# Kernel tuning notes

Hardware: AMD Instinct MI355X
Metric: run time of the kernel (lower is better)

Reference implementation:

```python
import jax, jax.numpy as jnp
import numpy as np

# Dimensions
B, C, H, W = 4, 256, 64, 64
O = 256                      # out_channels
K = 3                        # kernel size
K2 = K * K
STRIDE = (1, 1)
PAD = 1
Ho = (H + 2 * PAD - K) // STRIDE[0] + 1   # 64
Wo = (W + 2 * PAD - K) // STRIDE[1] + 1   # 64


def setup_inputs() -> dict:
    key = jax.random.key(0)
    ks = jax.random.split(key, 5)
    x = jax.random.normal(ks[0], (B, C, H, W), jnp.float32)
    # NOTE: the torch module zero-inits offset/modulator convs; we use small
    # random weights so the deformable sampling path is actually exercised.
    offset_w = 0.02 * jax.random.normal(ks[1], (2 * K2, C, K, K), jnp.float32)
    offset_b = jnp.zeros((2 * K2,), jnp.float32)
    mod_w = 0.02 * jax.random.normal(ks[2], (K2, C, K, K), jnp.float32)
    mod_b = jnp.zeros((K2,), jnp.float32)
    weight = jax.random.normal(ks[3], (O, C, K, K), jnp.float32) / np.sqrt(C * K2)
    return {"x": x, "offset_w": offset_w, "offset_b": offset_b,
            "mod_w": mod_w, "mod_b": mod_b, "weight": weight}


def _conv(x, w, b):
    y = jax.lax.conv_general_dilated(
        x, w, window_strides=STRIDE, padding=[(PAD, PAD), (PAD, PAD)],
        dimension_numbers=("NCHW", "OIHW", "NCHW"))
    return y + b[None, :, None, None]


def _deform_conv2d(x, offset, mask, weight):
    """Modulated deformable conv v2 (torchvision semantics, zero padding)."""
    Bq, Cq, Hq, Wq = x.shape
    # offset channels are (dy, dx) pairs per kernel tap, row-major over kernel
    off = offset.reshape(Bq, K2, 2, Ho, Wo)
    ky, kx = jnp.meshgrid(jnp.arange(K), jnp.arange(K), indexing="ij")
    ky = ky.reshape(K2).astype(x.dtype)
    kx = kx.reshape(K2).astype(x.dtype)
    hy = (jnp.arange(Ho) * STRIDE[0] - PAD).astype(x.dtype)
    wx = (jnp.arange(Wo) * STRIDE[1] - PAD).astype(x.dtype)
    # sampling positions [B, K2, Ho, Wo]
    py = off[:, :, 0] + ky[None, :, None, None] + hy[None, None, :, None]
    px = off[:, :, 1] + kx[None, :, None, None] + wx[None, None, None, :]

    P = K2 * Ho * Wo
    xf = x.reshape(Bq, Cq, Hq * Wq)
    y0 = jnp.floor(py)
    x0 = jnp.floor(px)
    val = jnp.zeros((Bq, Cq, P), x.dtype)
    for dy in (0.0, 1.0):
        for dx in (0.0, 1.0):
            yc = y0 + dy
            xc = x0 + dx
            wgt = (1.0 - jnp.abs(py - yc)) * (1.0 - jnp.abs(px - xc))
            valid = (yc >= 0) & (yc < Hq) & (xc >= 0) & (xc < Wq)
            idx = (jnp.clip(yc, 0, Hq - 1) * Wq
                   + jnp.clip(xc, 0, Wq - 1)).astype(jnp.int32).reshape(Bq, P)
            g = jnp.take_along_axis(xf, idx[:, None, :], axis=2)  # [B,C,P]
            val = val + (wgt * valid.astype(x.dtype)).reshape(Bq, 1, P) * g
    # modulation mask is per kernel tap, shared across channels
    cols = (val * mask.reshape(Bq, 1, P)).reshape(Bq, Cq, K2, Ho * Wo)
    out = jnp.einsum("bckp,ock->bop", cols, weight.reshape(weight.shape[0], Cq, K2))
    return out.reshape(Bq, weight.shape[0], Ho, Wo)


def reference(x, offset_w, offset_b, mod_w, mod_b, weight):
    offset = _conv(x, offset_w, offset_b)
    mask = 2.0 * jax.nn.sigmoid(_conv(x, mod_w, mod_b))
    return _deform_conv2d(x, offset, mask, weight)
```

## Files before the change

kernel.cpp:

```cpp
#include <hip/hip_runtime.h>
#include <math.h>


constexpr int Bn = 4;
constexpr int Cn = 256;
constexpr int Hn = 64;
constexpr int Wn = 64;
constexpr int On = 256;
constexpr int PB = Hn * Wn;
constexpr int NCH = 27;

typedef __attribute__((ext_vector_type(8))) _Float16 f16x8;
typedef __attribute__((ext_vector_type(2))) _Float16 f16x2;
typedef __attribute__((ext_vector_type(4))) float f32x4;

union FragU { uint4 u; f16x8 h; };

__device__ inline ushort f2h(float f) {
    _Float16 h = (_Float16)f;
    return __builtin_bit_cast(ushort, h);
}
__device__ inline uint pkh(float a, float b) {
    return __builtin_bit_cast(uint, __builtin_amdgcn_cvt_pkrtz(a, b));
}
__device__ inline f16x2 u2h(uint u) { return __builtin_bit_cast(f16x2, u); }
__device__ inline uint h2u(f16x2 h) { return __builtin_bit_cast(uint, h); }

__global__ __launch_bounds__(256)
void nhwcpack_kernel(const float* __restrict__ x,
                     const float* __restrict__ w,
                     const float* __restrict__ offw,
                     const float* __restrict__ modw,
                     ushort* __restrict__ xhf,
                     ushort* __restrict__ wTb,
                     ushort* __restrict__ owf)
{
    const int bid = blockIdx.x;
    const int b = bid >> 7, seg = bid & 127;
    const int t = threadIdx.x;
    __shared__ float tile[32][257];

    const float* src = x + (size_t)b * Cn * PB + seg * 32;
    #pragma unroll 4
    for (int i = 0; i < 32; ++i) {
        const int idx = i * 256 + t;
        const int c = idx >> 5, p = idx & 31;
        tile[p][c] = src[(size_t)c * PB + p];
    }
    __syncthreads();

    const int pr = t & 127;
    const int r0 = (t >> 7) * 16;
    uint* dH = reinterpret_cast<uint*>(xhf + ((size_t)b * PB + seg * 32) * 256);
    #pragma unroll 4
    for (int i = 0; i < 16; ++i) {
        const int row = r0 + i;
        const float v0 = tile[row][2 * pr];
        const float v1 = tile[row][2 * pr + 1];
        dH[(size_t)row * 128 + pr] = pkh(v0, v1);
    }

    #pragma unroll 1
    for (int u = 0; u < 5; ++u) {
        int unit = (u < 4) ? bid * 4 + u : (bid < 256 ? 2048 + bid : -1);
        if (unit < 0) break;
        const int tap = unit >> 8, c = unit & 255;
        const int o = t;
        wTb[((size_t)(unit >> 3) * 256 + o) * 8 + (c & 7)] =
            f2h(w[((size_t)o * Cn + c) * 9 + tap]);
        if (o < 32) {
            float v = 0.f;
            if (o < 18)      v = offw[((size_t)o * Cn + c) * 9 + tap];
            else if (o < 27) v = modw[((size_t)(o - 18) * Cn + c) * 9 + tap];
            owf[((size_t)(unit >> 3) * 32 + o) * 8 + (c & 7)] = f2h(v);
        }
    }
}

__global__ __launch_bounds__(512, 1)
void offmask_tile_kernel(const ushort* __restrict__ xhf,
                         const float* __restrict__ offb,
                         const float* __restrict__ modb,
                         const ushort* __restrict__ owf,
                         float* __restrict__ offm)
{
    const int hw = blockIdx.x;
    const int blk = (hw & 7) * 32 + (hw >> 3);
    const int b = blk >> 6, row = blk & 63;
    const int t = threadIdx.x;
    const int lane = t & 63;
    const int wv  = t >> 6;
    const int l15 = lane & 15;
    const int g   = lane >> 4;
    const int mt  = wv >> 2;
    const int nt  = wv & 3;

    __shared__ ushort xt[3 * 66 * 256];
    uint4* lds4 = reinterpret_cast<uint4*>(xt);

    {
        const int c  = t >> 3;
        const int og = (t & 7) * 4;
        #pragma unroll 1
        for (int r = 0; r < 3; ++r) {
            const int ysrc = row - 1 + r;
            const int ci = c + 1;
            const int base = (r * 66 + ci) * 32;
            if (ysrc >= 0 && ysrc < Hn) {
                const uint4* src = reinterpret_cast<const uint4*>(
                    xhf + ((size_t)(b * PB + ysrc * 64 + c)) * 256);
                #pragma unroll
                for (int j = 0; j < 4; ++j) {
                    const int o = og + j;
                    lds4[base + (o ^ (ci & 7))] = src[o];
                }
            } else {
                const uint4 z = make_uint4(0u, 0u, 0u, 0u);
                #pragma unroll
                for (int j = 0; j < 4; ++j) {
                    const int o = og + j;
                    lds4[base + (o ^ (ci & 7))] = z;
                }
            }
        }
        if (t < 192) {
            const int r = t >> 6, idx = t & 63;
            const int ci = (idx >= 32) ? 65 : 0;
            const int o = idx & 31;
            lds4[(r * 66 + ci) * 32 + (o ^ (ci & 7))] =
                make_uint4(0u, 0u, 0u, 0u);
        }
    }
    __syncthreads();

    const uint4* owfV = reinterpret_cast<const uint4*>(owf);
    f32x4 acc = (f32x4){0.f, 0.f, 0.f, 0.f};
    const int pos = nt * 16 + l15;

    #pragma unroll 1
    for (int tap = 0; tap < 9; ++tap) {
        const int ty = tap / 3, tx = tap % 3;
        const int ci = pos + tx;
        const int cbase = (ty * 66 + ci) * 32;
        const int cx = ci & 7;

        uint4 aH[8];
        #pragma unroll
        for (int s = 0; s < 8; ++s) {
            const size_t kb = (size_t)((tap * 8 + s) * 4 + g) * 32 + mt * 16 + l15;
            aH[s] = owfV[kb];
        }

        #pragma unroll
        for (int s = 0; s < 8; ++s) {
            FragU aHH, bH;
            aHH.u = aH[s];
            bH.u = lds4[cbase + ((4 * s + g) ^ cx)];
            acc = __builtin_amdgcn_mfma_f32_16x16x32_f16(aHH.h, bH.h, acc, 0, 0, 0);
        }
    }

    #pragma unroll
    for (int j = 0; j < 4; ++j) {
        const int ch = mt * 16 + g * 4 + j;
        if (ch < NCH) {
            float v = acc[j];
            if (ch < 18) v += offb[ch];
            else         v = 2.f / (1.f + expf(-(v + modb[ch - 18])));
            offm[((size_t)(b * NCH + ch)) * PB + row * 64 + pos] = v;
        }
    }
}

__global__ __launch_bounds__(512, 1)
void deform_nhwc_kernel(const ushort* __restrict__ xhf,
                        const float* __restrict__ offm,
                        const ushort* __restrict__ wTb,
                        float* __restrict__ out)
{
    const int hw = blockIdx.x;
    const int blk = (hw & 7) * 32 + (hw >> 3);
    const int b = blk >> 6, row = blk & 63;
    const int p0 = row * 64;
    const int t = threadIdx.x;
    const int lane = t & 63;
    const int wv  = t >> 6;
    const int l15 = lane & 15;
    const int g   = lane >> 4;

    __shared__ int4  s_off[576];
    __shared__ uint4 s_wgt[576];
    __shared__ uint  cols[2][4][1024];

    for (int ti = t; ti < 576; ti += 512) {
        const int k = ti >> 6, pos = ti & 63;
        const int p = p0 + pos;
        const float dy = offm[((size_t)(b * NCH + 2 * k)) * PB + p];
        const float dx = offm[((size_t)(b * NCH + 2 * k + 1)) * PB + p];
        const float m  = offm[((size_t)(b * NCH + 18 + k)) * PB + p];
        const int ky = k / 3, kx = k % 3;
        const float py = dy + (float)(ky + row - 1);
        const float px = dx + (float)(kx + pos - 1);
        const float y0f = floorf(py), x0f = floorf(px);
        const float fy = py - y0f, fx = px - x0f;
        const int y0 = (int)y0f, x0i = (int)x0f;
        const int y1 = y0 + 1, x1 = x0i + 1;
        const bool vy0 = (y0 >= 0) && (y0 < Hn);
        const bool vy1 = (y1 >= 0) && (y1 < Hn);
        const bool vx0 = (x0i >= 0) && (x0i < Wn);
        const bool vx1 = (x1 >= 0) && (x1 < Wn);
        const int y0c = min(max(y0, 0), Hn - 1);
        const int y1c = min(max(y1, 0), Hn - 1);
        const int x0c = min(max(x0i, 0), Wn - 1);
        const int x1c = min(max(x1, 0), Wn - 1);
        s_off[ti] = make_int4(y0c * Wn + x0c, y0c * Wn + x1c,
                              y1c * Wn + x0c, y1c * Wn + x1c);
        const float w0 = (vy0 && vx0) ? (1.f - fy) * (1.f - fx) * m : 0.f;
        const float w1 = (vy0 && vx1) ? (1.f - fy) * fx * m : 0.f;
        const float w2 = (vy1 && vx0) ? fy * (1.f - fx) * m : 0.f;
        const float w3 = (vy1 && vx1) ? fy * fx * m : 0.f;
        s_wgt[ti] = make_uint4(pkh(w0, w0), pkh(w1, w1),
                               pkh(w2, w2), pkh(w3, w3));
    }
    __syncthreads();

    const ushort* xb = xhf + (size_t)b * PB * 256;
    const int posT = t >> 4;
    const int chq  = t & 15;
    const uint4* wvp = reinterpret_cast<const uint4*>(wTb);
    const int o0 = wv * 32;

    const int ws0 = posT * 16
        + 4 * ((chq >> 2) ^ (posT & 3) ^ ((posT >> 2) & 3)) + (chq & 3);

    int ri[4];
    #pragma unroll
    for (int nt = 0; nt < 4; ++nt) {
        const int p = nt * 16 + l15;
        ri[nt] = p * 4 + (g ^ (p & 3) ^ ((p >> 2) & 3));
    }

    f32x4 acc[2][4];
    #pragma unroll
    for (int ot = 0; ot < 2; ++ot)
        #pragma unroll
        for (int nt = 0; nt < 4; ++nt)
            acc[ot][nt] = (f32x4){0.f, 0.f, 0.f, 0.f};

    auto LOADA = [&](int cch, uint4 (&ap)[4][2]) {
        #pragma unroll
        for (int s = 0; s < 4; ++s) {
            const int kb = (cch * 4 + s) * 4 + g;
            ap[s][0] = wvp[(size_t)kb * 256 + o0 + l15];
            ap[s][1] = wvp[(size_t)kb * 256 + o0 + 16 + l15];
        }
    };

    auto ISSUE = [&](int cch, uint (&gg)[32]) {
        const int tap = cch >> 1, cc0 = (cch & 1) * 128;
        const int4 oA = s_off[tap * 64 + posT];
        const int4 oB = s_off[tap * 64 + posT + 32];
        const ushort* xc = xb + cc0 + 2 * chq;
        #pragma unroll
        for (int s = 0; s < 4; ++s) {
            const int so = s * 32;
            gg[s * 8 + 0] = *reinterpret_cast<const uint*>(xc + (size_t)oA.x * 256 + so);
            gg[s * 8 + 1] = *reinterpret_cast<const uint*>(xc + (size_t)oA.y * 256 + so);
            gg[s * 8 + 2] = *reinterpret_cast<const uint*>(xc + (size_t)oA.z * 256 + so);
            gg[s * 8 + 3] = *reinterpret_cast<const uint*>(xc + (size_t)oA.w * 256 + so);
            gg[s * 8 + 4] = *reinterpret_cast<const uint*>(xc + (size_t)oB.x * 256 + so);
            gg[s * 8 + 5] = *reinterpret_cast<const uint*>(xc + (size_t)oB.y * 256 + so);
            gg[s * 8 + 6] = *reinterpret_cast<const uint*>(xc + (size_t)oB.z * 256 + so);
            gg[s * 8 + 7] = *reinterpret_cast<const uint*>(xc + (size_t)oB.w * 256 + so);
        }
    };

    auto COMBINE = [&](int cch, const uint (&gg)[32], uint* cbuf) {
        const int tap = cch >> 1;
        const uint4 wgtA = s_wgt[tap * 64 + posT];
        const uint4 wgtB = s_wgt[tap * 64 + posT + 32];
        #pragma unroll
        for (int s = 0; s < 4; ++s) {
            f16x2 v = u2h(gg[s * 8 + 0]) * u2h(wgtA.x);
            v += u2h(gg[s * 8 + 1]) * u2h(wgtA.y);
            v += u2h(gg[s * 8 + 2]) * u2h(wgtA.z);
            v += u2h(gg[s * 8 + 3]) * u2h(wgtA.w);
            cbuf[s * 1024 + ws0] = h2u(v);
            f16x2 u = u2h(gg[s * 8 + 4]) * u2h(wgtB.x);
            u += u2h(gg[s * 8 + 5]) * u2h(wgtB.y);
            u += u2h(gg[s * 8 + 6]) * u2h(wgtB.z);
            u += u2h(gg[s * 8 + 7]) * u2h(wgtB.w);
            cbuf[s * 1024 + ws0 + 512] = h2u(u);
        }
    };

    auto MFMAS = [&](const uint* cbuf, const uint4 (&ap)[4][2]) {
        #pragma unroll
        for (int s = 0; s < 4; ++s) {
            FragU a0, a1, bf[4];
            a0.u = ap[s][0]; a1.u = ap[s][1];
            #pragma unroll
            for (int nt = 0; nt < 4; ++nt)
                bf[nt].u = reinterpret_cast<const uint4*>(cbuf + s * 1024)[ri[nt]];
            #pragma unroll
            for (int nt = 0; nt < 4; ++nt) {
                acc[0][nt] = __builtin_amdgcn_mfma_f32_16x16x32_f16(
                    a0.h, bf[nt].h, acc[0][nt], 0, 0, 0);
                acc[1][nt] = __builtin_amdgcn_mfma_f32_16x16x32_f16(
                    a1.h, bf[nt].h, acc[1][nt], 0, 0, 0);
            }
        }
    };

    uint  gA[32], gB[32];
    uint4 aA[4][2], aB[4][2];

    LOADA(0, aA);
    ISSUE(0, gA);
    #pragma unroll 1
    for (int jj = 0; jj < 9; ++jj) {
        LOADA(2 * jj + 1, aB);
        ISSUE(2 * jj + 1, gB);
        COMBINE(2 * jj, gA, &cols[0][0][0]);
        asm volatile("s_waitcnt lgkmcnt(0)" ::: "memory");
        __builtin_amdgcn_s_barrier();
        asm volatile("" ::: "memory");
        MFMAS(&cols[0][0][0], aA);

        if (jj < 8) {
            LOADA(2 * jj + 2, aA);
            ISSUE(2 * jj + 2, gA);
        }
        COMBINE(2 * jj + 1, gB, &cols[1][0][0]);
        asm volatile("s_waitcnt lgkmcnt(0)" ::: "memory");
        __builtin_amdgcn_s_barrier();
        asm volatile("" ::: "memory");
        MFMAS(&cols[1][0][0], aB);
    }

    float* ob = out + (size_t)b * On * PB;
    #pragma unroll
    for (int ot = 0; ot < 2; ++ot)
        #pragma unroll
        for (int nt = 0; nt < 4; ++nt)
            #pragma unroll
            for (int j = 0; j < 4; ++j)
                ob[((size_t)(o0 + ot * 16 + g * 4 + j)) * PB
                   + p0 + nt * 16 + l15] = acc[ot][nt][j];
}

extern "C" void kernel_launch(void* const* d_in, const int* in_sizes, int n_in,
                              void* d_out, int out_size, void* d_ws, size_t ws_size,
                              hipStream_t stream)
{
    const float* x    = (const float*)d_in[0];
    const float* offw = (const float*)d_in[1];
    const float* offb = (const float*)d_in[2];
    const float* modw = (const float*)d_in[3];
    const float* modb = (const float*)d_in[4];
    const float* wgt  = (const float*)d_in[5];
    float* out = (float*)d_out;

    char* ws = (char*)d_ws;
    float*  offm = (float*)ws;
    ushort* wTb  = (ushort*)(ws + 1769472);
    ushort* owf  = (ushort*)(ws + 2949120);
    ushort* xhf  = (ushort*)(ws + 3244032);

    nhwcpack_kernel<<<dim3(512), dim3(256), 0, stream>>>(
        x, wgt, offw, modw, xhf, wTb, owf);
    offmask_tile_kernel<<<dim3(256), dim3(512), 0, stream>>>(
        xhf, offb, modb, owf, offm);
    deform_nhwc_kernel<<<dim3(256), dim3(512), 0, stream>>>(
        xhf, offm, wTb, out);
}
```

Before: 61.98 us.

## Split deform kernel into gather-producer and MFMA-consumer wave groups

```diff
diff --git a/kernel.cpp b/kernel.cpp
--- a/kernel.cpp
+++ b/kernel.cpp
@@ -13,6 +13,7 @@
 typedef __attribute__((ext_vector_type(8))) _Float16 f16x8;
 typedef __attribute__((ext_vector_type(2))) _Float16 f16x2;
 typedef __attribute__((ext_vector_type(4))) float f32x4;
+typedef __attribute__((ext_vector_type(4))) uint  uint4v;
 
 union FragU { uint4 u; f16x8 h; };
 
@@ -172,11 +173,11 @@
     }
 }
 
-__global__ __launch_bounds__(512, 1)
-void deform_nhwc_kernel(const ushort* __restrict__ xhf,
-                        const float* __restrict__ offm,
-                        const ushort* __restrict__ wTb,
-                        float* __restrict__ out)
+__global__ __launch_bounds__(512, 2)
+void deform_ws_kernel(const ushort* __restrict__ xhf,
+                      const float* __restrict__ offm,
+                      const ushort* __restrict__ wTb,
+                      float* __restrict__ out)
 {
     const int hw = blockIdx.x;
     const int blk = (hw & 7) * 32 + (hw >> 3);
@@ -225,128 +226,135 @@
     __syncthreads();
 
     const ushort* xb = xhf + (size_t)b * PB * 256;
-    const int posT = t >> 4;
-    const int chq  = t & 15;
-    const uint4* wvp = reinterpret_cast<const uint4*>(wTb);
-    const int o0 = wv * 32;
-
-    const int ws0 = posT * 16
-        + 4 * ((chq >> 2) ^ (posT & 3) ^ ((posT >> 2) & 3)) + (chq & 3);
-
-    int ri[4];
-    #pragma unroll
-    for (int nt = 0; nt < 4; ++nt) {
-        const int p = nt * 16 + l15;
-        ri[nt] = p * 4 + (g ^ (p & 3) ^ ((p >> 2) & 3));
-    }
-
-    f32x4 acc[2][4];
-    #pragma unroll
-    for (int ot = 0; ot < 2; ++ot)
-        #pragma unroll
-        for (int nt = 0; nt < 4; ++nt)
-            acc[ot][nt] = (f32x4){0.f, 0.f, 0.f, 0.f};
-
-    auto LOADA = [&](int cch, uint4 (&ap)[4][2]) {
-        #pragma unroll
-        for (int s = 0; s < 4; ++s) {
-            const int kb = (cch * 4 + s) * 4 + g;
-            ap[s][0] = wvp[(size_t)kb * 256 + o0 + l15];
-            ap[s][1] = wvp[(size_t)kb * 256 + o0 + 16 + l15];
-        }
-    };
-
-    auto ISSUE = [&](int cch, uint (&gg)[32]) {
-        const int tap = cch >> 1, cc0 = (cch & 1) * 128;
-        const int4 oA = s_off[tap * 64 + posT];
-        const int4 oB = s_off[tap * 64 + posT + 32];
-        const ushort* xc = xb + cc0 + 2 * chq;
-        #pragma unroll
-        for (int s = 0; s < 4; ++s) {
-            const int so = s * 32;
-            gg[s * 8 + 0] = *reinterpret_cast<const uint*>(xc + (size_t)oA.x * 256 + so);
-            gg[s * 8 + 1] = *reinterpret_cast<const uint*>(xc + (size_t)oA.y * 256 + so);
-            gg[s * 8 + 2] = *reinterpret_cast<const uint*>(xc + (size_t)oA.z * 256 + so);
-            gg[s * 8 + 3] = *reinterpret_cast<const uint*>(xc + (size_t)oA.w * 256 + so);
-            gg[s * 8 + 4] = *reinterpret_cast<const uint*>(xc + (size_t)oB.x * 256 + so);
-            gg[s * 8 + 5] = *reinterpret_cast<const uint*>(xc + (size_t)oB.y * 256 + so);
-            gg[s * 8 + 6] = *reinterpret_cast<const uint*>(xc + (size_t)oB.z * 256 + so);
-            gg[s * 8 + 7] = *reinterpret_cast<const uint*>(xc + (size_t)oB.w * 256 + so);
-        }
-    };
-
-    auto COMBINE = [&](int cch, const uint (&gg)[32], uint* cbuf) {
-        const int tap = cch >> 1;
-        const uint4 wgtA = s_wgt[tap * 64 + posT];
-        const uint4 wgtB = s_wgt[tap * 64 + posT + 32];
-        #pragma unroll
-        for (int s = 0; s < 4; ++s) {
-            f16x2 v = u2h(gg[s * 8 + 0]) * u2h(wgtA.x);
-            v += u2h(gg[s * 8 + 1]) * u2h(wgtA.y);
-            v += u2h(gg[s * 8 + 2]) * u2h(wgtA.z);
-            v += u2h(gg[s * 8 + 3]) * u2h(wgtA.w);
-            cbuf[s * 1024 + ws0] = h2u(v);
-            f16x2 u = u2h(gg[s * 8 + 4]) * u2h(wgtB.x);
-            u += u2h(gg[s * 8 + 5]) * u2h(wgtB.y);
-            u += u2h(gg[s * 8 + 6]) * u2h(wgtB.z);
-            u += u2h(gg[s * 8 + 7]) * u2h(wgtB.w);
-            cbuf[s * 1024 + ws0 + 512] = h2u(u);
-        }
-    };
-
-    auto MFMAS = [&](const uint* cbuf, const uint4 (&ap)[4][2]) {
-        #pragma unroll
-        for (int s = 0; s < 4; ++s) {
-            FragU a0, a1, bf[4];
-            a0.u = ap[s][0]; a1.u = ap[s][1];
+
+    if (wv < 4) {
+        const int chq  = t & 15;
+        const int posT = t >> 4;
+        const int sIdx = chq >> 2;
+        const int grp  = (chq & 3) ^ (posT & 3) ^ ((posT >> 2) & 3);
+        const int w4a  = posT * 4 + grp;
+        const ushort* xq = xb + 8 * chq;
+
+        auto PISSUE = [&](int cch, uint4v (&gg)[4][4]) {
+            const int tap = cch >> 1;
+            const ushort* xcc = xq + (cch & 1) * 128;
+            #pragma unroll
+            for (int u = 0; u < 4; ++u) {
+                const int4 o = s_off[tap * 64 + posT + u * 16];
+                gg[u][0] = *reinterpret_cast<const uint4v*>(xcc + (size_t)o.x * 256);
+                gg[u][1] = *reinterpret_cast<const uint4v*>(xcc + (size_t)o.y * 256);
+                gg[u][2] = *reinterpret_cast<const uint4v*>(xcc + (size_t)o.z * 256);
+                gg[u][3] = *reinterpret_cast<const uint4v*>(xcc + (size_t)o.w * 256);
+            }
+        };
+
+        auto PCOMBINE = [&](int cch, const uint4v (&gg)[4][4], uint* cbuf) {
+            const int tap = cch >> 1;
+            uint4v* dst = reinterpret_cast<uint4v*>(cbuf + sIdx * 1024);
+            #pragma unroll
+            for (int u = 0; u < 4; ++u) {
+                const uint4 wq = s_wgt[tap * 64 + posT + u * 16];
+                uint pr[4];
+                #pragma unroll
+                for (int j = 0; j < 4; ++j) {
+                    f16x2 v = u2h(gg[u][0][j]) * u2h(wq.x);
+                    v += u2h(gg[u][1][j]) * u2h(wq.y);
+                    v += u2h(gg[u][2][j]) * u2h(wq.z);
+                    v += u2h(gg[u][3][j]) * u2h(wq.w);
+                    pr[j] = h2u(v);
+                }
+                dst[w4a + u * 64] = (uint4v){pr[0], pr[1], pr[2], pr[3]};
+            }
+        };
+
+        uint4v gA[4][4], gB[4][4];
+        PISSUE(0, gA);
+        #pragma unroll 1
+        for (int jj = 0; jj < 9; ++jj) {
+            PISSUE(2 * jj + 1, gB);
+            PCOMBINE(2 * jj, gA, &cols[0][0][0]);
+            asm volatile("s_waitcnt lgkmcnt(0)" ::: "memory");
+            __builtin_amdgcn_s_barrier();
+            asm volatile("" ::: "memory");
+            if (jj < 8) PISSUE(2 * jj + 2, gA);
+            PCOMBINE(2 * jj + 1, gB, &cols[1][0][0]);
+            asm volatile("s_waitcnt lgkmcnt(0)" ::: "memory");
+            __builtin_amdgcn_s_barrier();
+            asm volatile("" ::: "memory");
+        }
+    } else {
+        const int cw = wv - 4;
+        const int o0 = cw * 64;
+        const uint4* wvp = reinterpret_cast<const uint4*>(wTb);
+
+        int ri[4];
+        #pragma unroll
+        for (int nt = 0; nt < 4; ++nt) {
+            const int p = nt * 16 + l15;
+            ri[nt] = p * 4 + (g ^ (p & 3) ^ ((p >> 2) & 3));
+        }
+
+        f32x4 acc[4][4];
+        #pragma unroll
+        for (int i = 0; i < 4; ++i)
             #pragma unroll
             for (int nt = 0; nt < 4; ++nt)
-                bf[nt].u = reinterpret_cast<const uint4*>(cbuf + s * 1024)[ri[nt]];
-            #pragma unroll
-            for (int nt = 0; nt < 4; ++nt) {
-                acc[0][nt] = __builtin_amdgcn_mfma_f32_16x16x32_f16(
-                    a0.h, bf[nt].h, acc[0][nt], 0, 0, 0);
-                acc[1][nt] = __builtin_amdgcn_mfma_f32_16x16x32_f16(
-                    a1.h, bf[nt].h, acc[1][nt], 0, 0, 0);
-            }
-        }
-    };
-
-    uint  gA[32], gB[32];
-    uint4 aA[4][2], aB[4][2];
-
-    LOADA(0, aA);
-    ISSUE(0, gA);
-    #pragma unroll 1
-    for (int jj = 0; jj < 9; ++jj) {
-        LOADA(2 * jj + 1, aB);
-        ISSUE(2 * jj + 1, gB);
-        COMBINE(2 * jj, gA, &cols[0][0][0]);
-        asm volatile("s_waitcnt lgkmcnt(0)" ::: "memory");
-        __builtin_amdgcn_s_barrier();
-        asm volatile("" ::: "memory");
-        MFMAS(&cols[0][0][0], aA);
-
-        if (jj < 8) {
-            LOADA(2 * jj + 2, aA);
-            ISSUE(2 * jj + 2, gA);
-        }
-        COMBINE(2 * jj + 1, gB, &cols[1][0][0]);
-        asm volatile("s_waitcnt lgkmcnt(0)" ::: "memory");
-        __builtin_amdgcn_s_barrier();
-        asm volatile("" ::: "memory");
-        MFMAS(&cols[1][0][0], aB);
-    }
-
-    float* ob = out + (size_t)b * On * PB;
-    #pragma unroll
-    for (int ot = 0; ot < 2; ++ot)
-        #pragma unroll
-        for (int nt = 0; nt < 4; ++nt)
-            #pragma unroll
-            for (int j = 0; j < 4; ++j)
-                ob[((size_t)(o0 + ot * 16 + g * 4 + j)) * PB
-                   + p0 + nt * 16 + l15] = acc[ot][nt][j];
+                acc[i][nt] = (f32x4){0.f, 0.f, 0.f, 0.f};
+
+        auto CLOADA = [&](int cch, uint4 (&ap)[4][4]) {
+            #pragma unroll
+            for (int s = 0; s < 4; ++s) {
+                const int kb = (cch * 4 + s) * 4 + g;
+                #pragma unroll
+                for (int i = 0; i < 4; ++i)
+                    ap[s][i] = wvp[(size_t)kb * 256 + o0 + i * 16 + l15];
+            }
+        };
+
+        auto CMFMA = [&](const uint* cbuf, const uint4 (&ap)[4][4]) {
+            __builtin_amdgcn_s_setprio(1);
+            #pragma unroll
+            for (int s = 0; s < 4; ++s) {
+                FragU a[4], bf[4];
+                #pragma unroll
+                for (int i = 0; i < 4; ++i) a[i].u = ap[s][i];
+                #pragma unroll
+                for (int nt = 0; nt < 4; ++nt)
+                    bf[nt].u = reinterpret_cast<const uint4*>(cbuf + s * 1024)[ri[nt]];
+                #pragma unroll
+                for (int i = 0; i < 4; ++i)
+                    #pragma unroll
+                    for (int nt = 0; nt < 4; ++nt)
+                        acc[i][nt] = __builtin_amdgcn_mfma_f32_16x16x32_f16(
+                            a[i].h, bf[nt].h, acc[i][nt], 0, 0, 0);
+            }
+            __builtin_amdgcn_s_setprio(0);
+        };
+
+        uint4 aA[4][4], aB[4][4];
+        CLOADA(0, aA);
+        #pragma unroll 1
+        for (int jj = 0; jj < 9; ++jj) {
+            __builtin_amdgcn_s_barrier();
+            asm volatile("" ::: "memory");
+            CLOADA(2 * jj + 1, aB);
+            CMFMA(&cols[0][0][0], aA);
+            __builtin_amdgcn_s_barrier();
+            asm volatile("" ::: "memory");
+            if (jj < 8) CLOADA(2 * jj + 2, aA);
+            CMFMA(&cols[1][0][0], aB);
+        }
+
+        float* ob = out + (size_t)b * On * PB;
+        #pragma unroll
+        for (int i = 0; i < 4; ++i)
+            #pragma unroll
+            for (int nt = 0; nt < 4; ++nt)
+                #pragma unroll
+                for (int j = 0; j < 4; ++j)
+                    ob[((size_t)(o0 + i * 16 + g * 4 + j)) * PB
+                       + p0 + nt * 16 + l15] = acc[i][nt][j];
+    }
 }
 
 extern "C" void kernel_launch(void* const* d_in, const int* in_sizes, int n_in,
@@ -371,6 +379,6 @@
         x, wgt, offw, modw, xhf, wTb, owf);
     offmask_tile_kernel<<<dim3(256), dim3(512), 0, stream>>>(
         xhf, offb, modb, owf, offm);
-    deform_nhwc_kernel<<<dim3(256), dim3(512), 0, stream>>>(
+    deform_ws_kernel<<<dim3(256), dim3(512), 0, stream>>>(
         xhf, offm, wTb, out);
 }
```

New measurement: 57.03 us. 8.0% less time.
